# Performance work log

Measured on AMD Instinct MI355X. Metric: run time of the kernel, lower is better.

The kernel has to match this reference:

```python
import jax, jax.numpy as jnp
import numpy as np

B, D, OUT = 256, 63, 128
DP = D + 1  # 64


def setup_inputs() -> dict:
    key = jax.random.key(0)
    k1, k2, k3, k4, k5 = jax.random.split(key, 5)
    return {
        "x": jax.random.normal(k1, (B, D), dtype=jnp.float32),
        "protein_output": jax.random.normal(k2, (B, D), dtype=jnp.float32),
        "dynamic_output": jax.random.normal(k3, (B, D), dtype=jnp.float32),
        "W": jax.random.normal(k4, (DP ** 3, OUT), dtype=jnp.float32) * 0.02,
        "b": jax.random.normal(k5, (OUT,), dtype=jnp.float32) * 0.02,
    }


def reference(x, protein_output, dynamic_output, W, b):
    bsz = x.shape[0]
    ones = jnp.ones((bsz, 1), dtype=x.dtype)
    a = jnp.concatenate([x, ones], axis=1)               # [B, D+1]
    p = jnp.concatenate([protein_output, ones], axis=1)   # [B, D+1]
    d = jnp.concatenate([dynamic_output, ones], axis=1)   # [B, D+1]
    # rank-1 trilinear outer product, flattened row-major: idx = (i*(D+1)+j)*(D+1)+k
    ab = jnp.einsum('bi,bj->bij', a, p)                   # [B, D+1, D+1]
    abc = jnp.einsum('bij,bk->bijk', ab, d)               # [B, D+1, D+1, D+1]
    feat = abc.reshape(bsz, -1)                           # [B, (D+1)^3]
    return feat @ W + b                                   # [B, OUT]
```

## Files before the change

### kernel.cpp

```cpp
#include <hip/hip_runtime.h>
#include <hip/hip_bf16.h>

typedef __attribute__((ext_vector_type(8))) short short8v;
typedef __attribute__((ext_vector_type(4))) float floatx4;

union Frag { uint4 u; short8v v; };

__device__ __forceinline__ unsigned int pkbf(float a, float b) {
  __hip_bfloat162 h = __float22bfloat162_rn(make_float2(a, b));
  union { __hip_bfloat162 h; unsigned int u; } c; c.h = h;
  return c.u;
}

__global__ void bias_init(const float* __restrict__ bias, float* __restrict__ out) {
  int idx = blockIdx.x * 256 + threadIdx.x;
  out[idx] = bias[idx & 127];
}

__global__ __launch_bounds__(128)
void reduce_k(const float* __restrict__ part, const float* __restrict__ bias,
              float* __restrict__ out) {
  int o = blockIdx.x * 128 + threadIdx.x;
  const float* p = part + o;
  float s0 = 0.f, s1 = 0.f, s2 = 0.f, s3 = 0.f;
  #pragma unroll 8
  for (int c = 0; c < 256; c += 4) {
    s0 += p[(long)c * 32768];
    s1 += p[(long)(c + 1) * 32768];
    s2 += p[(long)(c + 2) * 32768];
    s3 += p[(long)(c + 3) * 32768];
  }
  out[o] = s0 + s1 + s2 + s3 + bias[o & 127];
}

__global__ __launch_bounds__(512)
void conv_w(const float* __restrict__ W, uint4* __restrict__ Wb) {
  const int s_abs = blockIdx.x;
  const int q = threadIdx.x >> 7;
  const int col = threadIdx.x & 127;
  const float* src = W + (long)(s_abs * 32 + q * 8) * 128 + col;
  float w[8];
  #pragma unroll
  for (int t = 0; t < 8; ++t)
    w[t] = __builtin_nontemporal_load(src + t * 128);
  uint4 f;
  f.x = pkbf(w[0], w[1]);
  f.y = pkbf(w[2], w[3]);
  f.z = pkbf(w[4], w[5]);
  f.w = pkbf(w[6], w[7]);
  Wb[((long)s_abs * 4 + q) * 128 + col] = f;
}

__global__ __launch_bounds__(512, 2)
void tfn_gemm_bf(const float* __restrict__ X, const float* __restrict__ P,
                 const float* __restrict__ Dyn, const uint4* __restrict__ Wb,
                 float* __restrict__ part) {
  __shared__ float p_lds[16][256];

  const int tid = threadIdx.x;
  const int wv = tid >> 6, lane = tid & 63;
  const int q = lane >> 4, l16 = lane & 15;
  const int r = wv & 3;
  const int cg = wv >> 2;

  const int c = blockIdx.x;
  const int i = c >> 2;
  const int j0 = (c & 3) << 4;

  for (int idx = tid; idx < 256 * 16; idx += 512) {
    int bb = idx >> 4, jj = idx & 15;
    int j = j0 + jj;
    p_lds[jj][bb] = (j < 63) ? P[bb * 63 + j] : 1.0f;
  }

  float e[4][2][8];
  #pragma unroll
  for (int rt = 0; rt < 4; ++rt) {
    int brow = (r << 6) + (rt << 4) + l16;
    float av = (i < 63) ? X[brow * 63 + i] : 1.0f;
    #pragma unroll
    for (int h = 0; h < 2; ++h) {
      int kb = (h << 5) + (q << 3);
      #pragma unroll
      for (int t = 0; t < 8; ++t) {
        int k = kb + t;
        float dv = (k < 63) ? Dyn[brow * 63 + k] : 1.0f;
        e[rt][h][t] = av * dv;
      }
    }
  }

  floatx4 acc[4][4];
  #pragma unroll
  for (int a = 0; a < 4; ++a)
    #pragma unroll
    for (int b = 0; b < 4; ++b) acc[a][b] = (floatx4)0.0f;

  __syncthreads();

  const uint4* wb = Wb + ((long)(c * 128 + q) * 128) + (cg << 6) + l16;

  Frag wA[4], wB[4];

  #pragma unroll
  for (int nt = 0; nt < 4; ++nt)
    wA[nt].u = wb[nt * 16];

  for (int jj = 0; jj < 16; ++jj) {
    float pb[4];
    #pragma unroll
    for (int rt = 0; rt < 4; ++rt)
      pb[rt] = p_lds[jj][(r << 6) + (rt << 4) + l16];

    {
      #pragma unroll
      for (int nt = 0; nt < 4; ++nt)
        wB[nt].u = wb[(2 * jj + 1) * 512 + nt * 16];

      union { short8v v; unsigned int u[4]; } fa[4];
      #pragma unroll
      for (int rt = 0; rt < 4; ++rt)
        #pragma unroll
        for (int v2 = 0; v2 < 4; ++v2)
          fa[rt].u[v2] = pkbf(pb[rt] * e[rt][0][2 * v2], pb[rt] * e[rt][0][2 * v2 + 1]);
      #pragma unroll
      for (int rt = 0; rt < 4; ++rt)
        #pragma unroll
        for (int nt = 0; nt < 4; ++nt)
          acc[rt][nt] = __builtin_amdgcn_mfma_f32_16x16x32_bf16(
              fa[rt].v, wA[nt].v, acc[rt][nt], 0, 0, 0);
    }

    {
      if (jj < 15) {
        #pragma unroll
        for (int nt = 0; nt < 4; ++nt)
          wA[nt].u = wb[(2 * jj + 2) * 512 + nt * 16];
      }

      union { short8v v; unsigned int u[4]; } fa[4];
      #pragma unroll
      for (int rt = 0; rt < 4; ++rt)
        #pragma unroll
        for (int v2 = 0; v2 < 4; ++v2)
          fa[rt].u[v2] = pkbf(pb[rt] * e[rt][1][2 * v2], pb[rt] * e[rt][1][2 * v2 + 1]);
      #pragma unroll
      for (int rt = 0; rt < 4; ++rt)
        #pragma unroll
        for (int nt = 0; nt < 4; ++nt)
          acc[rt][nt] = __builtin_amdgcn_mfma_f32_16x16x32_bf16(
              fa[rt].v, wB[nt].v, acc[rt][nt], 0, 0, 0);
    }
  }

  float* pt = part + ((long)c << 15);
  #pragma unroll
  for (int rt = 0; rt < 4; ++rt)
    #pragma unroll
    for (int nt = 0; nt < 4; ++nt) {
      int col = (cg << 6) + (nt << 4) + l16;
      #pragma unroll
      for (int g = 0; g < 4; ++g) {
        int brow = (r << 6) + (rt << 4) + (q << 2) + g;
        pt[brow * 128 + col] = acc[rt][nt][g];
      }
    }
}

__global__ __launch_bounds__(512, 2)
void tfn_gemm(const float* __restrict__ X, const float* __restrict__ P,
              const float* __restrict__ Dyn, const float* __restrict__ W,
              float* __restrict__ part, float* __restrict__ out, int use_ws) {
  __shared__ float p_lds[16][256];

  const int tid = threadIdx.x;
  const int wv = tid >> 6, lane = tid & 63;
  const int q = lane >> 4, l16 = lane & 15;
  const int r = wv & 3;
  const int cg = wv >> 2;

  const int c = blockIdx.x;
  const int i = c >> 2;
  const int j0 = (c & 3) << 4;
  const long gk0 = (long)c << 10;

  for (int idx = tid; idx < 256 * 16; idx += 512) {
    int bb = idx >> 4, jj = idx & 15;
    int j = j0 + jj;
    p_lds[jj][bb] = (j < 63) ? P[bb * 63 + j] : 1.0f;
  }

  float e[4][2][8];
  #pragma unroll
  for (int rt = 0; rt < 4; ++rt) {
    int brow = (r << 6) + (rt << 4) + l16;
    float av = (i < 63) ? X[brow * 63 + i] : 1.0f;
    #pragma unroll
    for (int h = 0; h < 2; ++h) {
      int kb = (h << 5) + (q << 3);
      #pragma unroll
      for (int t = 0; t < 8; ++t) {
        int k = kb + t;
        float dv = (k < 63) ? Dyn[brow * 63 + k] : 1.0f;
        e[rt][h][t] = av * dv;
      }
    }
  }

  floatx4 acc[4][4];
  #pragma unroll
  for (int a = 0; a < 4; ++a)
    #pragma unroll
    for (int b = 0; b < 4; ++b) acc[a][b] = (floatx4)0.0f;

  __syncthreads();

  const float* wstep = W + (gk0 + (q << 3)) * 128 + (cg << 6) + l16;

  float wA[4][8], wB[4][8];

  #pragma unroll
  for (int nt = 0; nt < 4; ++nt)
    #pragma unroll
    for (int t = 0; t < 8; ++t)
      wA[nt][t] = wstep[t * 128 + nt * 16];

  for (int jj = 0; jj < 16; ++jj) {
    float pb[4];
    #pragma unroll
    for (int rt = 0; rt < 4; ++rt)
      pb[rt] = p_lds[jj][(r << 6) + (rt << 4) + l16];

    {
      const float* wp = wstep + ((long)(2 * jj + 1) << 12);
      #pragma unroll
      for (int nt = 0; nt < 4; ++nt)
        #pragma unroll
        for (int t = 0; t < 8; ++t)
          wB[nt][t] = wp[t * 128 + nt * 16];

      union { short8v v; unsigned int u[4]; } fb[4], fa[4];
      #pragma unroll
      for (int nt = 0; nt < 4; ++nt)
        #pragma unroll
        for (int v2 = 0; v2 < 4; ++v2)
          fb[nt].u[v2] = pkbf(wA[nt][2 * v2], wA[nt][2 * v2 + 1]);
      #pragma unroll
      for (int rt = 0; rt < 4; ++rt)
        #pragma unroll
        for (int v2 = 0; v2 < 4; ++v2)
          fa[rt].u[v2] = pkbf(pb[rt] * e[rt][0][2 * v2], pb[rt] * e[rt][0][2 * v2 + 1]);
      #pragma unroll
      for (int rt = 0; rt < 4; ++rt)
        #pragma unroll
        for (int nt = 0; nt < 4; ++nt)
          acc[rt][nt] = __builtin_amdgcn_mfma_f32_16x16x32_bf16(
              fa[rt].v, fb[nt].v, acc[rt][nt], 0, 0, 0);
    }

    {
      if (jj < 15) {
        const float* wp = wstep + ((long)(2 * jj + 2) << 12);
        #pragma unroll
        for (int nt = 0; nt < 4; ++nt)
          #pragma unroll
          for (int t = 0; t < 8; ++t)
            wA[nt][t] = wp[t * 128 + nt * 16];
      }

      union { short8v v; unsigned int u[4]; } fb[4], fa[4];
      #pragma unroll
      for (int nt = 0; nt < 4; ++nt)
        #pragma unroll
        for (int v2 = 0; v2 < 4; ++v2)
          fb[nt].u[v2] = pkbf(wB[nt][2 * v2], wB[nt][2 * v2 + 1]);
      #pragma unroll
      for (int rt = 0; rt < 4; ++rt)
        #pragma unroll
        for (int v2 = 0; v2 < 4; ++v2)
          fa[rt].u[v2] = pkbf(pb[rt] * e[rt][1][2 * v2], pb[rt] * e[rt][1][2 * v2 + 1]);
      #pragma unroll
      for (int rt = 0; rt < 4; ++rt)
        #pragma unroll
        for (int nt = 0; nt < 4; ++nt)
          acc[rt][nt] = __builtin_amdgcn_mfma_f32_16x16x32_bf16(
              fa[rt].v, fb[nt].v, acc[rt][nt], 0, 0, 0);
    }
  }

  if (use_ws) {
    float* pt = part + ((long)c << 15);
    #pragma unroll
    for (int rt = 0; rt < 4; ++rt)
      #pragma unroll
      for (int nt = 0; nt < 4; ++nt) {
        int col = (cg << 6) + (nt << 4) + l16;
        #pragma unroll
        for (int g = 0; g < 4; ++g) {
          int brow = (r << 6) + (rt << 4) + (q << 2) + g;
          pt[brow * 128 + col] = acc[rt][nt][g];
        }
      }
  } else {
    #pragma unroll
    for (int rt = 0; rt < 4; ++rt)
      #pragma unroll
      for (int nt = 0; nt < 4; ++nt) {
        int col = (cg << 6) + (nt << 4) + l16;
        #pragma unroll
        for (int g = 0; g < 4; ++g) {
          int brow = (r << 6) + (rt << 4) + (q << 2) + g;
          atomicAdd(&out[brow * 128 + col], acc[rt][nt][g]);
        }
      }
  }
}

extern "C" void kernel_launch(void* const* d_in, const int* in_sizes, int n_in,
                              void* d_out, int out_size, void* d_ws, size_t ws_size,
                              hipStream_t stream) {
  const float* x   = (const float*)d_in[0];
  const float* p   = (const float*)d_in[1];
  const float* dyn = (const float*)d_in[2];
  const float* W   = (const float*)d_in[3];
  const float* b   = (const float*)d_in[4];
  float* out = (float*)d_out;

  const size_t wb_bytes   = (size_t)262144 * 128 * 2;
  const size_t part_bytes = (size_t)256 * 32768 * sizeof(float);
  const size_t need_new   = wb_bytes + part_bytes;
  const size_t need_old   = part_bytes;

  if (d_ws != nullptr && ws_size >= need_new) {
    uint4* Wb   = (uint4*)d_ws;
    float* part = (float*)((char*)d_ws + wb_bytes);
    conv_w<<<8192, 512, 0, stream>>>(W, Wb);
    tfn_gemm_bf<<<256, 512, 0, stream>>>(x, p, dyn, Wb, part);
    reduce_k<<<256, 128, 0, stream>>>(part, b, out);
  } else if (d_ws != nullptr && ws_size >= need_old) {
    float* part = (float*)d_ws;
    tfn_gemm<<<256, 512, 0, stream>>>(x, p, dyn, W, part, out, 1);
    reduce_k<<<256, 128, 0, stream>>>(part, b, out);
  } else {
    bias_init<<<128, 256, 0, stream>>>(b, out);
    tfn_gemm<<<256, 512, 0, stream>>>(x, p, dyn, W, nullptr, out, 0);
  }
}
```

Baseline: 252.9 us.

## Stream fp32 W through double-buffered LDS in GEMM, drop separate bf16 conversion pass

Removes the separate conv_w kernel that rewrote W as bf16 in workspace. The GEMM now reads fp32 W directly with coalesced 16-byte nontemporal loads into registers, stages them into padded double-buffered LDS tiles, and converts to bf16 when building MFMA fragments. This cuts total W traffic (no extra write plus reread of a bf16 copy) at the cost of per-step LDS traffic and block barriers. The reduction kernel also splits the 256 partials across four thread groups per output column and combines them through shared memory.

```diff
diff --git a/kernel.cpp b/kernel.cpp
--- a/kernel.cpp
+++ b/kernel.cpp
@@ -3,8 +3,7 @@
 
 typedef __attribute__((ext_vector_type(8))) short short8v;
 typedef __attribute__((ext_vector_type(4))) float floatx4;
-
-union Frag { uint4 u; short8v v; };
+typedef __attribute__((ext_vector_type(4))) unsigned int uint4v;
 
 __device__ __forceinline__ unsigned int pkbf(float a, float b) {
   __hip_bfloat162 h = __float22bfloat162_rn(make_float2(a, b));
@@ -17,44 +16,38 @@
   out[idx] = bias[idx & 127];
 }
 
-__global__ __launch_bounds__(128)
-void reduce_k(const float* __restrict__ part, const float* __restrict__ bias,
-              float* __restrict__ out) {
-  int o = blockIdx.x * 128 + threadIdx.x;
-  const float* p = part + o;
+__global__ __launch_bounds__(512)
+void reduce_v3(const float* __restrict__ part, const float* __restrict__ bias,
+               float* __restrict__ out) {
+  const int tid = threadIdx.x;
+  const int o = tid & 127;
+  const int qr = tid >> 7;
+  const int og = blockIdx.x * 128 + o;
+
+  const float* pp = part + (((long)(qr * 64)) << 15) + og;
   float s0 = 0.f, s1 = 0.f, s2 = 0.f, s3 = 0.f;
-  #pragma unroll 8
-  for (int c = 0; c < 256; c += 4) {
-    s0 += p[(long)c * 32768];
-    s1 += p[(long)(c + 1) * 32768];
-    s2 += p[(long)(c + 2) * 32768];
-    s3 += p[(long)(c + 3) * 32768];
-  }
-  out[o] = s0 + s1 + s2 + s3 + bias[o & 127];
-}
-
-__global__ __launch_bounds__(512)
-void conv_w(const float* __restrict__ W, uint4* __restrict__ Wb) {
-  const int s_abs = blockIdx.x;
-  const int q = threadIdx.x >> 7;
-  const int col = threadIdx.x & 127;
-  const float* src = W + (long)(s_abs * 32 + q * 8) * 128 + col;
-  float w[8];
-  #pragma unroll
-  for (int t = 0; t < 8; ++t)
-    w[t] = __builtin_nontemporal_load(src + t * 128);
-  uint4 f;
-  f.x = pkbf(w[0], w[1]);
-  f.y = pkbf(w[2], w[3]);
-  f.z = pkbf(w[4], w[5]);
-  f.w = pkbf(w[6], w[7]);
-  Wb[((long)s_abs * 4 + q) * 128 + col] = f;
+  #pragma unroll 4
+  for (int n = 0; n < 64; n += 4) {
+    s0 += __builtin_nontemporal_load(pp + ((long)n << 15));
+    s1 += __builtin_nontemporal_load(pp + ((long)(n + 1) << 15));
+    s2 += __builtin_nontemporal_load(pp + ((long)(n + 2) << 15));
+    s3 += __builtin_nontemporal_load(pp + ((long)(n + 3) << 15));
+  }
+  float sum = (s0 + s1) + (s2 + s3);
+
+  __shared__ float red[3][128];
+  if (qr) red[qr - 1][o] = sum;
+  __syncthreads();
+  if (qr == 0)
+    out[og] = sum + red[0][o] + red[1][o] + red[2][o] + bias[o];
 }
 
 __global__ __launch_bounds__(512, 2)
-void tfn_gemm_bf(const float* __restrict__ X, const float* __restrict__ P,
-                 const float* __restrict__ Dyn, const uint4* __restrict__ Wb,
+void tfn_gemm_v3(const float* __restrict__ X, const float* __restrict__ P,
+                 const float* __restrict__ Dyn, const float* __restrict__ W,
                  float* __restrict__ part) {
+  __shared__ __align__(16) float wt0[4160];
+  __shared__ __align__(16) float wt1[4160];
   __shared__ float p_lds[16][256];
 
   const int tid = threadIdx.x;
@@ -67,6 +60,11 @@
   const int i = c >> 2;
   const int j0 = (c & 3) << 4;
 
+  const uint4v* wsrc = (const uint4v*)(W + (((long)c) << 10) * 128);
+
+  uint4v rg0 = __builtin_nontemporal_load(&wsrc[tid]);
+  uint4v rg1 = __builtin_nontemporal_load(&wsrc[512 + tid]);
+
   for (int idx = tid; idx < 256 * 16; idx += 512) {
     int bb = idx >> 4, jj = idx & 15;
     int j = j0 + jj;
@@ -90,34 +88,54 @@
     }
   }
 
+  const int Lf0 = tid << 2;
+  const int Lf1 = (tid + 512) << 2;
+  const int d0 = Lf0 + ((Lf0 >> 8) << 2);
+  const int d1 = Lf1 + ((Lf1 >> 8) << 2);
+
+  *(uint4v*)&wt0[d0] = rg0;
+  *(uint4v*)&wt0[d1] = rg1;
+  rg0 = __builtin_nontemporal_load(&wsrc[1024 + tid]);
+  rg1 = __builtin_nontemporal_load(&wsrc[1536 + tid]);
+
   floatx4 acc[4][4];
   #pragma unroll
   for (int a = 0; a < 4; ++a)
     #pragma unroll
     for (int b = 0; b < 4; ++b) acc[a][b] = (floatx4)0.0f;
 
+  const int wbase = q * 1040 + (cg << 6) + l16;
+  const int prow = (r << 6) + l16;
+
   __syncthreads();
-
-  const uint4* wb = Wb + ((long)(c * 128 + q) * 128) + (cg << 6) + l16;
-
-  Frag wA[4], wB[4];
-
-  #pragma unroll
-  for (int nt = 0; nt < 4; ++nt)
-    wA[nt].u = wb[nt * 16];
 
   for (int jj = 0; jj < 16; ++jj) {
     float pb[4];
     #pragma unroll
     for (int rt = 0; rt < 4; ++rt)
-      pb[rt] = p_lds[jj][(r << 6) + (rt << 4) + l16];
+      pb[rt] = p_lds[jj][prow + (rt << 4)];
 
     {
-      #pragma unroll
-      for (int nt = 0; nt < 4; ++nt)
-        wB[nt].u = wb[(2 * jj + 1) * 512 + nt * 16];
-
-      union { short8v v; unsigned int u[4]; } fa[4];
+      *(uint4v*)&wt1[d0] = rg0;
+      *(uint4v*)&wt1[d1] = rg1;
+      if (jj < 15) {
+        rg0 = __builtin_nontemporal_load(&wsrc[(2 * jj + 2) * 1024 + tid]);
+        rg1 = __builtin_nontemporal_load(&wsrc[(2 * jj + 2) * 1024 + 512 + tid]);
+      }
+
+      float w[4][8];
+      #pragma unroll
+      for (int nt = 0; nt < 4; ++nt)
+        #pragma unroll
+        for (int t = 0; t < 8; ++t)
+          w[nt][t] = wt0[wbase + (nt << 4) + t * 128 + ((t >> 1) << 2)];
+
+      union { short8v v; unsigned int u[4]; } fb[4], fa[4];
+      #pragma unroll
+      for (int nt = 0; nt < 4; ++nt)
+        #pragma unroll
+        for (int v2 = 0; v2 < 4; ++v2)
+          fb[nt].u[v2] = pkbf(w[nt][2 * v2], w[nt][2 * v2 + 1]);
       #pragma unroll
       for (int rt = 0; rt < 4; ++rt)
         #pragma unroll
@@ -128,17 +146,32 @@
         #pragma unroll
         for (int nt = 0; nt < 4; ++nt)
           acc[rt][nt] = __builtin_amdgcn_mfma_f32_16x16x32_bf16(
-              fa[rt].v, wA[nt].v, acc[rt][nt], 0, 0, 0);
+              fa[rt].v, fb[nt].v, acc[rt][nt], 0, 0, 0);
+
+      __syncthreads();
     }
 
     {
       if (jj < 15) {
-        #pragma unroll
-        for (int nt = 0; nt < 4; ++nt)
-          wA[nt].u = wb[(2 * jj + 2) * 512 + nt * 16];
-      }
-
-      union { short8v v; unsigned int u[4]; } fa[4];
+        *(uint4v*)&wt0[d0] = rg0;
+        *(uint4v*)&wt0[d1] = rg1;
+        rg0 = __builtin_nontemporal_load(&wsrc[(2 * jj + 3) * 1024 + tid]);
+        rg1 = __builtin_nontemporal_load(&wsrc[(2 * jj + 3) * 1024 + 512 + tid]);
+      }
+
+      float w[4][8];
+      #pragma unroll
+      for (int nt = 0; nt < 4; ++nt)
+        #pragma unroll
+        for (int t = 0; t < 8; ++t)
+          w[nt][t] = wt1[wbase + (nt << 4) + t * 128 + ((t >> 1) << 2)];
+
+      union { short8v v; unsigned int u[4]; } fb[4], fa[4];
+      #pragma unroll
+      for (int nt = 0; nt < 4; ++nt)
+        #pragma unroll
+        for (int v2 = 0; v2 < 4; ++v2)
+          fb[nt].u[v2] = pkbf(w[nt][2 * v2], w[nt][2 * v2 + 1]);
       #pragma unroll
       for (int rt = 0; rt < 4; ++rt)
         #pragma unroll
@@ -149,7 +182,9 @@
         #pragma unroll
         for (int nt = 0; nt < 4; ++nt)
           acc[rt][nt] = __builtin_amdgcn_mfma_f32_16x16x32_bf16(
-              fa[rt].v, wB[nt].v, acc[rt][nt], 0, 0, 0);
+              fa[rt].v, fb[nt].v, acc[rt][nt], 0, 0, 0);
+
+      if (jj < 15) __syncthreads();
     }
   }
 
@@ -170,7 +205,7 @@
 __global__ __launch_bounds__(512, 2)
 void tfn_gemm(const float* __restrict__ X, const float* __restrict__ P,
               const float* __restrict__ Dyn, const float* __restrict__ W,
-              float* __restrict__ part, float* __restrict__ out, int use_ws) {
+              float* __restrict__ out) {
   __shared__ float p_lds[16][256];
 
   const int tid = threadIdx.x;
@@ -218,7 +253,6 @@
   const float* wstep = W + (gk0 + (q << 3)) * 128 + (cg << 6) + l16;
 
   float wA[4][8], wB[4][8];
-
   #pragma unroll
   for (int nt = 0; nt < 4; ++nt)
     #pragma unroll
@@ -288,32 +322,17 @@
     }
   }
 
-  if (use_ws) {
-    float* pt = part + ((long)c << 15);
-    #pragma unroll
-    for (int rt = 0; rt < 4; ++rt)
-      #pragma unroll
-      for (int nt = 0; nt < 4; ++nt) {
-        int col = (cg << 6) + (nt << 4) + l16;
-        #pragma unroll
-        for (int g = 0; g < 4; ++g) {
-          int brow = (r << 6) + (rt << 4) + (q << 2) + g;
-          pt[brow * 128 + col] = acc[rt][nt][g];
-        }
-      }
-  } else {
-    #pragma unroll
-    for (int rt = 0; rt < 4; ++rt)
-      #pragma unroll
-      for (int nt = 0; nt < 4; ++nt) {
-        int col = (cg << 6) + (nt << 4) + l16;
-        #pragma unroll
-        for (int g = 0; g < 4; ++g) {
-          int brow = (r << 6) + (rt << 4) + (q << 2) + g;
-          atomicAdd(&out[brow * 128 + col], acc[rt][nt][g]);
-        }
-      }
-  }
+  #pragma unroll
+  for (int rt = 0; rt < 4; ++rt)
+    #pragma unroll
+    for (int nt = 0; nt < 4; ++nt) {
+      int col = (cg << 6) + (nt << 4) + l16;
+      #pragma unroll
+      for (int g = 0; g < 4; ++g) {
+        int brow = (r << 6) + (rt << 4) + (q << 2) + g;
+        atomicAdd(&out[brow * 128 + col], acc[rt][nt][g]);
+      }
+    }
 }
 
 extern "C" void kernel_launch(void* const* d_in, const int* in_sizes, int n_in,
@@ -326,23 +345,14 @@
   const float* b   = (const float*)d_in[4];
   float* out = (float*)d_out;
 
-  const size_t wb_bytes   = (size_t)262144 * 128 * 2;
   const size_t part_bytes = (size_t)256 * 32768 * sizeof(float);
-  const size_t need_new   = wb_bytes + part_bytes;
-  const size_t need_old   = part_bytes;
-
-  if (d_ws != nullptr && ws_size >= need_new) {
-    uint4* Wb   = (uint4*)d_ws;
-    float* part = (float*)((char*)d_ws + wb_bytes);
-    conv_w<<<8192, 512, 0, stream>>>(W, Wb);
-    tfn_gemm_bf<<<256, 512, 0, stream>>>(x, p, dyn, Wb, part);
-    reduce_k<<<256, 128, 0, stream>>>(part, b, out);
-  } else if (d_ws != nullptr && ws_size >= need_old) {
+
+  if (d_ws != nullptr && ws_size >= part_bytes) {
     float* part = (float*)d_ws;
-    tfn_gemm<<<256, 512, 0, stream>>>(x, p, dyn, W, part, out, 1);
-    reduce_k<<<256, 128, 0, stream>>>(part, b, out);
+    tfn_gemm_v3<<<256, 512, 0, stream>>>(x, p, dyn, W, part);
+    reduce_v3<<<256, 512, 0, stream>>>(part, b, out);
   } else {
     bias_init<<<128, 256, 0, stream>>>(b, out);
-    tfn_gemm<<<256, 512, 0, stream>>>(x, p, dyn, W, nullptr, out, 0);
-  }
-}
+    tfn_gemm<<<256, 512, 0, stream>>>(x, p, dyn, W, out);
+  }
+}
```

Result: faster. 226.5 us (-10.4%).
